# Kernel tuning notes

Hardware: AMD Instinct MI355X
Metric: run time of the kernel (lower is better)

Reference implementation:

```python
import jax, jax.numpy as jnp
import numpy as np

N_HEADS = 16
N_KV = 8
HEAD_DIM = 128
HID = 2048
GROUPS = N_HEADS // N_KV
THETA = 10000.0


def _rope_cos_sin(position_ids, dtype):
    # position_ids: [1, S] int
    inv_freq = 1.0 / (THETA ** (jnp.arange(0, HEAD_DIM, 2, dtype=jnp.float32) / HEAD_DIM))
    freqs = position_ids.astype(jnp.float32)[:, :, None] * inv_freq[None, None, :]  # [1,S,hd/2]
    emb = jnp.concatenate([freqs, freqs], axis=-1)  # [1,S,hd]
    return jnp.cos(emb).astype(dtype)[:, None, :, :], jnp.sin(emb).astype(dtype)[:, None, :, :]


def _rotate_half(x):
    x1, x2 = x[..., : HEAD_DIM // 2], x[..., HEAD_DIM // 2 :]
    return jnp.concatenate([-x2, x1], axis=-1)


def setup_inputs() -> dict:
    key = jax.random.key(0)
    ks = jax.random.split(key, 8)
    B, S = 2, 2048
    hidden_states = jax.random.normal(ks[0], (B, S, HID), jnp.float32)
    Wq = jax.random.normal(ks[1], (HID, N_HEADS * HEAD_DIM), jnp.float32) * 0.02
    Wk = jax.random.normal(ks[2], (HID, N_KV * HEAD_DIM), jnp.float32) * 0.02
    Wv = jax.random.normal(ks[3], (HID, N_KV * HEAD_DIM), jnp.float32) * 0.02
    Wo = jax.random.normal(ks[4], (HID, HID), jnp.float32) * 0.02
    gate = jnp.zeros((1, N_HEADS, 1, 1), jnp.float32)
    memory_in = jax.random.normal(ks[5], (B, N_KV, HEAD_DIM, HEAD_DIM), jnp.float32)
    norm_in = jax.random.uniform(ks[6], (B, N_KV, 1, HEAD_DIM), jnp.float32)
    position_ids = jnp.arange(S, dtype=jnp.int32)[None, :]
    return {"hidden_states": hidden_states, "Wq": Wq, "Wk": Wk, "Wv": Wv, "Wo": Wo,
            "gate": gate, "memory_in": memory_in, "norm_in": norm_in,
            "position_ids": position_ids}


def reference(hidden_states, Wq, Wk, Wv, Wo, gate, memory_in, norm_in, position_ids):
    B, S, _ = hidden_states.shape
    # projections -> [B, H, S, hd]
    q = jnp.einsum('bsh,ho->bso', hidden_states, Wq).reshape(B, S, N_HEADS, HEAD_DIM).transpose(0, 2, 1, 3)
    k = jnp.einsum('bsh,ho->bso', hidden_states, Wk).reshape(B, S, N_KV, HEAD_DIM).transpose(0, 2, 1, 3)
    v = jnp.einsum('bsh,ho->bso', hidden_states, Wv).reshape(B, S, N_KV, HEAD_DIM).transpose(0, 2, 1, 3)

    # ---- compressive memory retrieval (pre-RoPE q, as in original) ----
    sigma_q = jax.nn.elu(q) + 1.0  # [B, nH, S, hd]
    mem_tiled = jnp.tile(memory_in, (1, GROUPS, 1, 1))          # torch .repeat tiles
    norm_tiled = jnp.tile(norm_in, (1, GROUPS, 1, 1))            # [B, nH, 1, hd]
    memory_output = jnp.einsum('bhsd,bhde->bhse', sigma_q, mem_tiled)
    norm_bcast = jnp.einsum('bhsd,bhd->bhs', sigma_q, norm_tiled[:, :, 0, :])[..., None]
    memory_output = memory_output / norm_bcast

    # ---- memory update (pre-RoPE k, v) ----
    sigma_k = jax.nn.elu(k) + 1.0  # [B, nKV, S, hd]
    updated_memory = memory_in + jnp.einsum('bhsd,bhse->bhde', sigma_k, v)
    updated_norm = norm_in + jnp.sum(sigma_k, axis=2, keepdims=True)

    # ---- RoPE ----
    cos, sin = _rope_cos_sin(position_ids, q.dtype)
    q = q * cos + _rotate_half(q) * sin
    k = k * cos + _rotate_half(k) * sin

    # ---- repeat_kv (interleave, groups) ----
    k = jnp.repeat(k, GROUPS, axis=1)
    v = jnp.repeat(v, GROUPS, axis=1)

    # ---- causal SDPA ----
    scale = 1.0 / np.sqrt(HEAD_DIM)
    scores = jnp.einsum('bhqd,bhkd->bhqk', q, k) * scale
    causal = jnp.tril(jnp.ones((S, S), dtype=bool))
    scores = jnp.where(causal[None, None], scores, jnp.finfo(scores.dtype).min)
    probs = jax.nn.softmax(scores, axis=-1)
    attn = jnp.einsum('bhqk,bhkd->bhqd', probs, v)

    # ---- gated combination + output projection ----
    g = jax.nn.sigmoid(gate)
    combined = g * memory_output + (1.0 - g) * attn  # [B, nH, S, hd]
    combined = combined.transpose(0, 2, 1, 3).reshape(B, S, HID)
    final_output = jnp.einsum('bsh,ho->bso', combined, Wo)
    return final_output, updated_memory, updated_norm
```

## Files before the change

### kernel.cpp

```cpp
#include <hip/hip_runtime.h>

#define BATCH 2
#define SEQ   2048
#define HID   2048
#define NH    16
#define NKV   8
#define HD    128
#define M_ROWS (BATCH * SEQ)
#define QKV_N  4096

typedef __attribute__((ext_vector_type(8))) __bf16 bf16x8;
typedef __attribute__((ext_vector_type(4))) float  f32x4;

static __device__ __forceinline__ f32x4 mfma16(bf16x8 a, bf16x8 b, f32x4 c) {
    return __builtin_amdgcn_mfma_f32_16x16x32_bf16(a, b, c, 0, 0, 0);
}
static __device__ __forceinline__ float sigma_f(float x) {
    return x > 0.f ? x + 1.f : __expf(x);
}
static __device__ __forceinline__ void gload16(const __bf16* g, __bf16* l) {
    __builtin_amdgcn_global_load_lds(
        (const __attribute__((address_space(1))) void*)g,
        (__attribute__((address_space(3))) void*)l, 16, 0, 0);
}

#define OFF_QKV  0ull
#define OFF_SQ   67108864ull
#define OFF_QR   83886080ull
#define OFF_KR   100663296ull
#define OFF_VT   109051904ull
#define OFF_ND   117440512ull
#define OFF_CB   117702656ull
#define OFF_PART 134479872ull
#define OFF_BND  142868480ull
#define OFF_MAXP 143130624ull
#define OFF_NPART 143134720ull
#define NSPLIT 8

__global__ void f2b_k(const float* __restrict__ src, __bf16* __restrict__ dst)
{
    const size_t i = ((size_t)blockIdx.x * 256 + threadIdx.x) * 8;
    const float4 v0 = *reinterpret_cast<const float4*>(src + i);
    const float4 v1 = *reinterpret_cast<const float4*>(src + i + 4);
    bf16x8 t;
    t[0]=(__bf16)v0.x; t[1]=(__bf16)v0.y; t[2]=(__bf16)v0.z; t[3]=(__bf16)v0.w;
    t[4]=(__bf16)v1.x; t[5]=(__bf16)v1.y; t[6]=(__bf16)v1.z; t[7]=(__bf16)v1.w;
    *reinterpret_cast<bf16x8*>(dst + i) = t;
}

__global__ __launch_bounds__(256) void tr_k(const float* __restrict__ W,
                                            __bf16* __restrict__ Bt, int K, int N)
{
    __shared__ __bf16 T[64][72];
    const int k0 = blockIdx.x * 64, n0 = blockIdx.y * 64;
    const int t = threadIdx.x;
    #pragma unroll
    for (int i = 0; i < 4; ++i) {
        const int idx = t + i * 256;
        const int r = idx >> 4, c4 = (idx & 15) * 4;
        const float4 v = *reinterpret_cast<const float4*>(&W[(size_t)(k0 + r) * N + n0 + c4]);
        T[c4 + 0][r] = (__bf16)v.x; T[c4 + 1][r] = (__bf16)v.y;
        T[c4 + 2][r] = (__bf16)v.z; T[c4 + 3][r] = (__bf16)v.w;
    }
    __syncthreads();
    #pragma unroll
    for (int i = 0; i < 2; ++i) {
        const int idx = t + i * 256;
        const int rr = idx >> 3, cc = (idx & 7) * 8;
        *reinterpret_cast<bf16x8*>(&Bt[(size_t)(n0 + rr) * K + k0 + cc]) =
            *reinterpret_cast<bf16x8*>(&T[rr][cc]);
    }
}

__global__ __launch_bounds__(512, 2) void gemm8_k(const __bf16* __restrict__ A,
                                                  const __bf16* __restrict__ Bt,
                                                  float* __restrict__ C,
                                                  int N, int K)
{
    __shared__ __align__(16) __bf16 smem[65536];
    const int tid = threadIdx.x, wave = tid >> 6, lane = tid & 63;
    const int l15 = lane & 15, l4 = lane >> 4;
    const int wr = wave >> 2, wc = wave & 3;

    const int nwg = gridDim.x;
    const int swz = (blockIdx.x & 7) * (nwg >> 3) + (blockIdx.x >> 3);
    const int NBN = N >> 8;
    const int bm = swz / NBN, bn = swz - bm * NBN;
    const int m0 = bm << 8, n0 = bn << 8;

    const int NKT = K >> 6;

    const int srow   = tid >> 2;
    const int schunk = (tid & 3) ^ ((tid >> 3) & 3);
    const int sdst   = wave * 512;

    const int achunk = l4 ^ ((l15 >> 1) & 3);
    const int aoff = (wr * 128 + l15) * 32 + achunk * 8;
    const int boff = (wc * 64  + l15) * 32 + achunk * 8;

    f32x4 acc[2][4][4] = {};
    bf16x8 af[4], bfr[4];

#define STAGE_SLAB(gb, r0, koff, slabptr) do {                                   \
        const __bf16* _g = (gb) + (size_t)((r0) + srow) * K + (koff) + schunk * 8; \
        gload16(_g,                    (slabptr) + sdst);                        \
        gload16(_g + (size_t)128 * K,  (slabptr) + sdst + 4096);                 \
    } while (0)

    STAGE_SLAB(A,  m0, 0,  smem);
    STAGE_SLAB(Bt, n0, 0,  smem + 16384);
    STAGE_SLAB(A,  m0, 32, smem + 8192);
    STAGE_SLAB(Bt, n0, 32, smem + 24576);
    STAGE_SLAB(A,  m0, 64, smem + 32768);
    STAGE_SLAB(Bt, n0, 64, smem + 32768 + 16384);
    asm volatile("s_waitcnt vmcnt(4)" ::: "memory");
    __builtin_amdgcn_s_barrier();

    #pragma unroll 1
    for (int T = 0; T < NKT; ++T) {
        __bf16* bufc = smem + (T & 1) * 32768;
        __bf16* bufn = smem + ((T & 1) ^ 1) * 32768;
        const int kt1 = (T + 1) * 64, kt2 = (T + 2) * 64;

        {
            const __bf16* As = bufc;
            const __bf16* Bs = bufc + 16384;
            #pragma unroll
            for (int f = 0; f < 4; ++f)  af[f]  = *reinterpret_cast<const bf16x8*>(As + aoff + f * 512);
            #pragma unroll
            for (int nf = 0; nf < 4; ++nf) bfr[nf] = *reinterpret_cast<const bf16x8*>(Bs + boff + nf * 512);
            if (T + 1 < NKT) STAGE_SLAB(A, m0, kt1 + 32, bufn + 8192);
            __builtin_amdgcn_s_barrier();
            __builtin_amdgcn_s_setprio(1);
            #pragma unroll
            for (int f = 0; f < 4; ++f)
                #pragma unroll
                for (int nf = 0; nf < 4; ++nf)
                    acc[0][f][nf] = mfma16(af[f], bfr[nf], acc[0][f][nf]);
            __builtin_amdgcn_s_setprio(0);
            __builtin_amdgcn_s_barrier();
        }
        {
            const __bf16* As = bufc;
            #pragma unroll
            for (int f = 0; f < 4; ++f)  af[f] = *reinterpret_cast<const bf16x8*>(As + aoff + 2048 + f * 512);
            if (T + 1 < NKT) STAGE_SLAB(Bt, n0, kt1 + 32, bufn + 24576);
            __builtin_amdgcn_s_barrier();
            __builtin_amdgcn_s_setprio(1);
            #pragma unroll
            for (int f = 0; f < 4; ++f)
                #pragma unroll
                for (int nf = 0; nf < 4; ++nf)
                    acc[1][f][nf] = mfma16(af[f], bfr[nf], acc[1][f][nf]);
            __builtin_amdgcn_s_setprio(0);
            __builtin_amdgcn_s_barrier();
        }
        {
            const __bf16* As = bufc + 8192;
            const __bf16* Bs = bufc + 24576;
            #pragma unroll
            for (int f = 0; f < 4; ++f)  af[f]  = *reinterpret_cast<const bf16x8*>(As + aoff + f * 512);
            #pragma unroll
            for (int nf = 0; nf < 4; ++nf) bfr[nf] = *reinterpret_cast<const bf16x8*>(Bs + boff + nf * 512);
            if (T + 2 < NKT) STAGE_SLAB(A, m0, kt2, bufc);
            __builtin_amdgcn_s_barrier();
            __builtin_amdgcn_s_setprio(1);
            #pragma unroll
            for (int f = 0; f < 4; ++f)
                #pragma unroll
                for (int nf = 0; nf < 4; ++nf)
                    acc[0][f][nf] = mfma16(af[f], bfr[nf], acc[0][f][nf]);
            __builtin_amdgcn_s_setprio(0);
            __builtin_amdgcn_s_barrier();
        }
        {
            const __bf16* As = bufc + 8192;
            #pragma unroll
            for (int f = 0; f < 4; ++f)  af[f] = *reinterpret_cast<const bf16x8*>(As + aoff + 2048 + f * 512);
            if (T + 2 < NKT) STAGE_SLAB(Bt, n0, kt2, bufc + 16384);
            __builtin_amdgcn_s_barrier();
            __builtin_amdgcn_s_setprio(1);
            #pragma unroll
            for (int f = 0; f < 4; ++f)
                #pragma unroll
                for (int nf = 0; nf < 4; ++nf)
                    acc[1][f][nf] = mfma16(af[f], bfr[nf], acc[1][f][nf]);
            __builtin_amdgcn_s_setprio(0);
            if (T < NKT - 2) asm volatile("s_waitcnt vmcnt(4)" ::: "memory");
            else             asm volatile("s_waitcnt vmcnt(0)" ::: "memory");
            __builtin_amdgcn_s_barrier();
        }
    }
#undef STAGE_SLAB

    #pragma unroll
    for (int mh = 0; mh < 2; ++mh)
        #pragma unroll
        for (int f = 0; f < 4; ++f)
            #pragma unroll
            for (int nf = 0; nf < 4; ++nf)
                #pragma unroll
                for (int r = 0; r < 4; ++r) {
                    const int row = m0 + wr * 128 + mh * 64 + f * 16 + l4 * 4 + r;
                    const int col = n0 + wc * 64 + nf * 16 + l15;
                    C[(size_t)row * N + col] = acc[mh][f][nf][r];
                }
}

__global__ __launch_bounds__(256) void prep_k(const float* __restrict__ qkv,
                                              const float* __restrict__ norm_in,
                                              const int* __restrict__ pos_ids,
                                              __bf16* __restrict__ sq, __bf16* __restrict__ qr,
                                              __bf16* __restrict__ kr, __bf16* __restrict__ vt,
                                              float* __restrict__ nd, float* __restrict__ bnd,
                                              float* __restrict__ maxp)
{
    const int sc = blockIdx.x, kvh = blockIdx.y, b = blockIdx.z;
    const int s0 = sc * 32, t = threadIdx.x;
    const float scale = 0.08838834764831845f;
    const float s2 = scale * scale;
    const float NEG_LN_TH = -0.14391156831212787f;
    __shared__ float krn[32];

    {
        const int row = t >> 2;
        const int head = row >> 5, sl = row & 31;
        const int hq = kvh * 2 + head, nh = hq & 7;
        const int dq = (t & 3) * 16;
        const int pos = pos_ids[s0 + sl];
        const float* qp = qkv + (size_t)(b * SEQ + s0 + sl) * QKV_N + hq * 128;
        const float* np = norm_in + (b * NKV + nh) * 128;

        float x0[16], x1[16];
        #pragma unroll
        for (int i = 0; i < 16; i += 4) {
            *reinterpret_cast<float4*>(&x0[i]) = *reinterpret_cast<const float4*>(qp + dq + i);
            *reinterpret_cast<float4*>(&x1[i]) = *reinterpret_cast<const float4*>(qp + dq + 64 + i);
        }
        float nds = 0.f, qns = 0.f;
        bf16x8 sqv0[2], sqv1[2], qrv0[2], qrv1[2];
        #pragma unroll
        for (int i = 0; i < 16; ++i) {
            const int j = dq + i;
            float c, sn;
            __sincosf((float)pos * __expf((float)j * NEG_LN_TH), &sn, &c);
            qrv0[i >> 3][i & 7] = (__bf16)((x0[i] * c - x1[i] * sn) * scale);
            qrv1[i >> 3][i & 7] = (__bf16)((x1[i] * c + x0[i] * sn) * scale);
            const float sg0 = sigma_f(x0[i]), sg1 = sigma_f(x1[i]);
            sqv0[i >> 3][i & 7] = (__bf16)sg0;
            sqv1[i >> 3][i & 7] = (__bf16)sg1;
            nds += sg0 * np[j] + sg1 * np[j + 64];
            qns += (x0[i] * x0[i] + x1[i] * x1[i]) * s2;
        }
        __bf16* sqp = sq + ((size_t)(b * NH + hq) * SEQ + s0 + sl) * 128;
        __bf16* qrp = qr + ((size_t)(b * NH + hq) * SEQ + s0 + sl) * 128;
        *reinterpret_cast<bf16x8*>(sqp + dq)      = sqv0[0];
        *reinterpret_cast<bf16x8*>(sqp + dq + 8)  = sqv0[1];
        *reinterpret_cast<bf16x8*>(sqp + dq + 64) = sqv1[0];
        *reinterpret_cast<bf16x8*>(sqp + dq + 72) = sqv1[1];
        *reinterpret_cast<bf16x8*>(qrp + dq)      = qrv0[0];
        *reinterpret_cast<bf16x8*>(qrp + dq + 8)  = qrv0[1];
        *reinterpret_cast<bf16x8*>(qrp + dq + 64) = qrv1[0];
        *reinterpret_cast<bf16x8*>(qrp + dq + 72) = qrv1[1];

        nds += __shfl_xor(nds, 1); nds += __shfl_xor(nds, 2);
        qns += __shfl_xor(qns, 1); qns += __shfl_xor(qns, 2);
        if ((t & 3) == 0) {
            nd [(size_t)(b * NH + hq) * SEQ + s0 + sl] = nds;
            bnd[(size_t)(b * NH + hq) * SEQ + s0 + sl] = qns;
        }
    }

    if (t < 128) {
        const int sl = t >> 2;
        const int dq = (t & 3) * 16;
        const int pos = pos_ids[s0 + sl];
        const float* kp = qkv + (size_t)(b * SEQ + s0 + sl) * QKV_N + 2048 + kvh * 128;
        float x0[16], x1[16];
        #pragma unroll
        for (int i = 0; i < 16; i += 4) {
            *reinterpret_cast<float4*>(&x0[i]) = *reinterpret_cast<const float4*>(kp + dq + i);
            *reinterpret_cast<float4*>(&x1[i]) = *reinterpret_cast<const float4*>(kp + dq + 64 + i);
        }
        bf16x8 kv0[2], kv1[2];
        float kns = 0.f;
        #pragma unroll
        for (int i = 0; i < 16; ++i) {
            const int j = dq + i;
            float c, sn;
            __sincosf((float)pos * __expf((float)j * NEG_LN_TH), &sn, &c);
            kv0[i >> 3][i & 7] = (__bf16)(x0[i] * c - x1[i] * sn);
            kv1[i >> 3][i & 7] = (__bf16)(x1[i] * c + x0[i] * sn);
            kns += x0[i] * x0[i] + x1[i] * x1[i];
        }
        __bf16* krp = kr + ((size_t)(b * NKV + kvh) * SEQ + s0 + sl) * 128;
        *reinterpret_cast<bf16x8*>(krp + dq)      = kv0[0];
        *reinterpret_cast<bf16x8*>(krp + dq + 8)  = kv0[1];
        *reinterpret_cast<bf16x8*>(krp + dq + 64) = kv1[0];
        *reinterpret_cast<bf16x8*>(krp + dq + 72) = kv1[1];
        kns += __shfl_xor(kns, 1); kns += __shfl_xor(kns, 2);
        if ((t & 3) == 0) krn[sl] = kns;
    }

    __shared__ float vl[128][33];
    {
        const int sl = t >> 3, dch = (t & 7) * 16;
        const float* vp = qkv + (size_t)(b * SEQ + s0 + sl) * QKV_N + 3072 + kvh * 128 + dch;
        float xv[16];
        #pragma unroll
        for (int i = 0; i < 16; i += 4)
            *reinterpret_cast<float4*>(&xv[i]) = *reinterpret_cast<const float4*>(vp + i);
        #pragma unroll
        for (int i = 0; i < 16; ++i) vl[dch + i][sl] = xv[i];
    }
    __syncthreads();
    if (t == 0) {
        float mx = 0.f;
        #pragma unroll
        for (int i = 0; i < 32; ++i) mx = fmaxf(mx, krn[i]);
        maxp[((b * NKV + kvh) << 6) + sc] = mx;
    }
    {
        const int d = t >> 1, sh = (t & 1) * 16;
        bf16x8 o0, o1;
        #pragma unroll
        for (int j = 0; j < 8; ++j) o0[j] = (__bf16)vl[d][sh + j];
        #pragma unroll
        for (int j = 0; j < 8; ++j) o1[j] = (__bf16)vl[d][sh + 8 + j];
        __bf16* vp = vt + ((size_t)((b * NKV + kvh) * 128 + d)) * SEQ + s0 + sh;
        *reinterpret_cast<bf16x8*>(vp)     = o0;
        *reinterpret_cast<bf16x8*>(vp + 8) = o1;
    }
}

__global__ __launch_bounds__(256) void memout_k(const __bf16* __restrict__ sq,
                                                const float* __restrict__ mem_in,
                                                const float* __restrict__ nd,
                                                const float* __restrict__ gate,
                                                __bf16* __restrict__ cb)
{
    __shared__ __align__(16) __bf16 mt[128][136];
    const int tid = threadIdx.x;
    const int h = blockIdx.y, b = blockIdx.z;
    const int s0 = blockIdx.x * 64;

    const float* mem = mem_in + (size_t)(b * NKV + (h & 7)) * 16384;
    for (int i = tid; i < 16384; i += 256) {
        int dd = i >> 7, e = i & 127;
        mt[e][dd] = (__bf16)mem[i];
    }
    __syncthreads();

    const int wave = tid >> 6, lane = tid & 63, l15 = lane & 15, l4 = lane >> 4;
    f32x4 acc[8] = {};
    const __bf16* sqb = sq + ((size_t)(b * NH + h) * SEQ + s0 + wave * 16 + l15) * 128;
    #pragma unroll
    for (int kb = 0; kb < 4; ++kb) {
        bf16x8 a = *reinterpret_cast<const bf16x8*>(sqb + kb * 32 + l4 * 8);
        #pragma unroll
        for (int nc = 0; nc < 8; ++nc) {
            bf16x8 bb = *reinterpret_cast<bf16x8*>(&mt[nc * 16 + l15][kb * 32 + l4 * 8]);
            acc[nc] = mfma16(a, bb, acc[nc]);
        }
    }
    float g = 1.f / (1.f + __expf(-gate[h]));
    #pragma unroll
    for (int r = 0; r < 4; ++r) {
        int srow = s0 + wave * 16 + l4 * 4 + r;
        float scl = g / nd[(size_t)(b * NH + h) * SEQ + srow];
        __bf16* cbp = cb + (size_t)(b * SEQ + srow) * HID + h * 128;
        #pragma unroll
        for (int nc = 0; nc < 8; ++nc)
            cbp[nc * 16 + l15] = (__bf16)(acc[nc][r] * scl);
    }
}

__global__ __launch_bounds__(256) void memupd_k(const float* __restrict__ qkv,
                                                float* __restrict__ part,
                                                float* __restrict__ npart)
{
    const int sp = blockIdx.x, h = blockIdx.y, b = blockIdx.z;
    const int tid = threadIdx.x;
    const int tx = tid & 15, ty = tid >> 4;
    __shared__ __align__(16) float sk[8][128];
    __shared__ __align__(16) float sv[8][128];
    float acc[8][8] = {};
    float nacc = 0.f;

    const int s0 = sp * (SEQ / NSPLIT);
    for (int so = 0; so < SEQ / NSPLIT; so += 8) {
        for (int i = tid; i < 8 * 128; i += 256) {
            int rr = i >> 7, dd = i & 127;
            const float* rowp = qkv + (size_t)(b * SEQ + s0 + so + rr) * QKV_N;
            sk[rr][dd] = sigma_f(rowp[2048 + h * 128 + dd]);
            sv[rr][dd] = rowp[3072 + h * 128 + dd];
        }
        __syncthreads();
        if (tid < 128) {
            #pragma unroll
            for (int rr = 0; rr < 8; ++rr) nacc += sk[rr][tid];
        }
        #pragma unroll
        for (int rr = 0; rr < 8; ++rr) {
            float4 k0 = *reinterpret_cast<float4*>(&sk[rr][tx * 8]);
            float4 k1 = *reinterpret_cast<float4*>(&sk[rr][tx * 8 + 4]);
            float4 v0 = *reinterpret_cast<float4*>(&sv[rr][ty * 8]);
            float4 v1 = *reinterpret_cast<float4*>(&sv[rr][ty * 8 + 4]);
            float kreg[8] = {k0.x,k0.y,k0.z,k0.w,k1.x,k1.y,k1.z,k1.w};
            float vreg[8] = {v0.x,v0.y,v0.z,v0.w,v1.x,v1.y,v1.z,v1.w};
            #pragma unroll
            for (int i = 0; i < 8; ++i)
                #pragma unroll
                for (int j2 = 0; j2 < 8; ++j2)
                    acc[i][j2] += kreg[i] * vreg[j2];
        }
        __syncthreads();
    }
    float* pb = part + ((size_t)sp * (BATCH * NKV) + b * NKV + h) * 16384;
    #pragma unroll
    for (int i = 0; i < 8; ++i)
        #pragma unroll
        for (int j2 = 0; j2 < 8; ++j2)
            pb[(tx * 8 + i) * 128 + ty * 8 + j2] = acc[i][j2];
    if (tid < 128)
        npart[((size_t)sp * (BATCH * NKV) + b * NKV + h) * 128 + tid] = nacc;
}

__global__ void memred_k(const float* __restrict__ part, const float* __restrict__ mem_in,
                         float* __restrict__ out_mem)
{
    const size_t i = (size_t)blockIdx.x * 256 + threadIdx.x;
    float a = mem_in[i];
    #pragma unroll
    for (int sp = 0; sp < NSPLIT; ++sp) a += part[(size_t)sp * 262144 + i];
    out_mem[i] = a;
}

__global__ void normred_k(const float* __restrict__ npart, const float* __restrict__ norm_in,
                          float* __restrict__ out_norm)
{
    const int bh = blockIdx.x, d = threadIdx.x;
    float a = norm_in[bh * 128 + d];
    #pragma unroll
    for (int sp = 0; sp < NSPLIT; ++sp)
        a += npart[((size_t)sp * (BATCH * NKV) + bh) * 128 + d];
    out_norm[bh * 128 + d] = a;
}

__global__ __launch_bounds__(256, 2) void attn_k(const __bf16* __restrict__ qr,
                                                 const __bf16* __restrict__ kr,
                                                 const __bf16* __restrict__ vt,
                                                 const float* __restrict__ gate,
                                                 const float* __restrict__ bnd,
                                                 const float* __restrict__ maxp,
                                                 __bf16* __restrict__ cb)
{
    __shared__ __align__(16) char smem[81920];
    __bf16* Ks   = (__bf16*)smem;
    __bf16* Vs   = (__bf16*)(smem + 32768);
    __bf16* plds = (__bf16*)(smem + 65536);
    float*  red  = (float*)smem;
    float*  lred = (float*)(smem + 65536);

    const int tid = threadIdx.x, wave = tid >> 6, lane = tid & 63;
    const int l15 = lane & 15, l4 = lane >> 4;

    const int n   = blockIdx.x + 16 * (blockIdx.y + 16 * blockIdx.z);
    const int xcd = n & 7, i64 = n >> 3;
    const int grp = xcd * 2 + (i64 >> 5);
    const int within = i64 & 31;
    const int b   = grp >> 3;
    const int kvh = grp & 7;
    const int h   = kvh * 2 + (within >> 4);
    const int x   = within & 15;

    const __bf16* kbase = kr + (size_t)(b * NKV + kvh) * SEQ * 128;
    const __bf16* vbase = vt + (size_t)(b * NKV + kvh) * 128 * SEQ;
    const float* bbase  = bnd + (size_t)(b * NH + h) * SEQ;

    const float g  = 1.f / (1.f + __expf(-gate[h]));
    const float gi = 1.f - g;
    float kn2 = 0.f;
    const float* mp = maxp + (b * NKV + kvh) * 64;
    #pragma unroll
    for (int i = 0; i < 64; i += 4) {
        const float4 v = *reinterpret_cast<const float4*>(mp + i);
        kn2 = fmaxf(kn2, fmaxf(fmaxf(v.x, v.y), fmaxf(v.z, v.w)));
    }
    const float knmax = sqrtf(kn2);

    bf16x8 ones;
    #pragma unroll
    for (int j = 0; j < 8; ++j) ones[j] = (__bf16)1.0f;

    const int srow = wave * 32 + (lane >> 4);
    __bf16* ksd = Ks + wave * 4096;
    __bf16* vsd = Vs + wave * 4096;

    __bf16* pw = plds + wave * 2048;
    const int ksub = wave >> 1;
    const int wq   = wave & 1;

    #pragma unroll 1
    for (int tile = 0; tile < 2; ++tile) {
        const int q0 = (tile == 0 ? x : 31 - x) * 64;
        const int qw = q0 + wq * 32;
        const int NT = (q0 >> 6) + 1;
        const int NI = (NT + 1) >> 1;

        bf16x8 af[2][4];
        float m_r[2][4];
        #pragma unroll
        for (int m = 0; m < 2; ++m) {
            const __bf16* qb = qr + ((size_t)(b * NH + h) * SEQ + qw + m * 16 + l15) * 128;
            #pragma unroll
            for (int kb = 0; kb < 4; ++kb)
                af[m][kb] = *reinterpret_cast<const bf16x8*>(qb + kb * 32 + l4 * 8);
            #pragma unroll
            for (int r = 0; r < 4; ++r)
                m_r[m][r] = sqrtf(bbase[qw + m * 16 + l4 * 4 + r]) * knmax + 1.0f;
        }

        f32x4 o0[8] = {}, o1[8] = {};
        f32x4 lc0 = {}, lc1 = {};

        #pragma unroll 1
        for (int it = 0; it < NI; ++it) {
            const int kt0 = it * 128;
            #pragma unroll
            for (int j = 0; j < 8; ++j) {
                const int row = srow + j * 4;
                const int ch  = (lane & 15) ^ (row & 7);
                gload16(kbase + (size_t)(kt0 + row) * 128 + ch * 8, ksd + j * 512);
                gload16(vbase + (size_t)row * SEQ + kt0 + ch * 8,   vsd + j * 512);
            }
            __syncthreads();

            const int s = 2 * it + ksub;
            if (s < NT) {
                const int krow0 = ksub * 64;
                f32x4 s0[4] = {}, s1[4] = {};
                #pragma unroll
                for (int kb = 0; kb < 4; ++kb) {
                    #pragma unroll
                    for (int sub = 0; sub < 4; ++sub) {
                        const int krow = krow0 + sub * 16 + l15;
                        bf16x8 bb = *reinterpret_cast<const bf16x8*>(
                            Ks + krow * 128 + (((kb * 4 + l4) ^ (krow & 7)) * 8));
                        s0[sub] = mfma16(af[0][kb], bb, s0[sub]);
                        s1[sub] = mfma16(af[1][kb], bb, s1[sub]);
                    }
                }
                #pragma unroll
                for (int r = 0; r < 4; ++r) {
                    const int q0r = qw + l4 * 4 + r;
                    const int q1r = q0r + 16;
                    const int p0r = l4 * 4 + r, p1r = p0r + 16;
                    #pragma unroll
                    for (int sub = 0; sub < 4; ++sub) {
                        const int key = s * 64 + sub * 16 + l15;
                        float p0 = __expf(s0[sub][r] - m_r[0][r]);
                        float p1 = __expf(s1[sub][r] - m_r[1][r]);
                        p0 = (key <= q0r) ? p0 : 0.f;
                        p1 = (key <= q1r) ? p1 : 0.f;
                        const int cc = (sub * 16 + l15) >> 3, cl = l15 & 7;
                        pw[p0r * 64 + ((cc ^ (p0r & 7)) * 8) + cl] = (__bf16)p0;
                        pw[p1r * 64 + ((cc ^ (p1r & 7)) * 8) + cl] = (__bf16)p1;
                    }
                }
                const int pr1 = 16 + l15;
                bf16x8 a00 = *reinterpret_cast<bf16x8*>(pw + l15 * 64 + ((l4 ^ (l15 & 7)) * 8));
                bf16x8 a01 = *reinterpret_cast<bf16x8*>(pw + l15 * 64 + (((4 + l4) ^ (l15 & 7)) * 8));
                bf16x8 a10 = *reinterpret_cast<bf16x8*>(pw + pr1 * 64 + ((l4 ^ (pr1 & 7)) * 8));
                bf16x8 a11 = *reinterpret_cast<bf16x8*>(pw + pr1 * 64 + (((4 + l4) ^ (pr1 & 7)) * 8));
                lc0 = mfma16(a00, ones, lc0); lc0 = mfma16(a01, ones, lc0);
                lc1 = mfma16(a10, ones, lc1); lc1 = mfma16(a11, ones, lc1);
                #pragma unroll
                for (int nc = 0; nc < 8; ++nc) {
                    const int vrow = nc * 16 + l15;
                    bf16x8 b0 = *reinterpret_cast<bf16x8*>(
                        Vs + vrow * 128 + (((ksub * 8 + l4) ^ (vrow & 7)) * 8));
                    bf16x8 b1 = *reinterpret_cast<bf16x8*>(
                        Vs + vrow * 128 + (((ksub * 8 + 4 + l4) ^ (vrow & 7)) * 8));
                    o0[nc] = mfma16(a00, b0, o0[nc]); o0[nc] = mfma16(a01, b1, o0[nc]);
                    o1[nc] = mfma16(a10, b0, o1[nc]); o1[nc] = mfma16(a11, b1, o1[nc]);
                }
            }
            __syncthreads();
        }

        if (wave >= 2) {
            float* rb = red + (wave - 2) * 4224;
            #pragma unroll
            for (int nc = 0; nc < 8; ++nc)
                #pragma unroll
                for (int r = 0; r < 4; ++r) {
                    rb[(l4 * 4 + r) * 132 + nc * 16 + l15]        = o0[nc][r];
                    rb[(16 + l4 * 4 + r) * 132 + nc * 16 + l15]   = o1[nc][r];
                }
            if (l15 == 0) {
                float* lb = lred + (wave - 2) * 32;
                #pragma unroll
                for (int r = 0; r < 4; ++r) {
                    lb[l4 * 4 + r]      = lc0[r];
                    lb[16 + l4 * 4 + r] = lc1[r];
                }
            }
        }
        __syncthreads();
        if (wave < 2) {
            float* rb = red + wave * 4224;
            const float* lb = lred + wave * 32;
            #pragma unroll
            for (int r = 0; r < 4; ++r) {
                const int qrow = qw + l4 * 4 + r;
                const float i0 = gi / (lc0[r] + lb[l4 * 4 + r]);
                const float i1 = gi / (lc1[r] + lb[16 + l4 * 4 + r]);
                __bf16* c0 = cb + (size_t)(b * SEQ + qrow) * HID + h * 128;
                __bf16* c1 = cb + (size_t)(b * SEQ + qrow + 16) * HID + h * 128;
                #pragma unroll
                for (int nc = 0; nc < 8; ++nc) {
                    const int dd = nc * 16 + l15;
                    const float v0 = o0[nc][r] + rb[(l4 * 4 + r) * 132 + dd];
                    const float v1 = o1[nc][r] + rb[(16 + l4 * 4 + r) * 132 + dd];
                    c0[dd] = (__bf16)((float)c0[dd] + v0 * i0);
                    c1[dd] = (__bf16)((float)c1[dd] + v1 * i1);
                }
            }
        }
        __syncthreads();
    }
}

extern "C" void kernel_launch(void* const* d_in, const int* in_sizes, int n_in,
                              void* d_out, int out_size, void* d_ws, size_t ws_size,
                              hipStream_t stream)
{
    const float* hidden  = (const float*)d_in[0];
    const float* Wq      = (const float*)d_in[1];
    const float* Wk      = (const float*)d_in[2];
    const float* Wv      = (const float*)d_in[3];
    const float* Wo      = (const float*)d_in[4];
    const float* gate    = (const float*)d_in[5];
    const float* mem_in  = (const float*)d_in[6];
    const float* norm_in = (const float*)d_in[7];
    const int*   pos     = (const int*)d_in[8];

    float* out_final = (float*)d_out;
    float* out_mem   = out_final + (size_t)BATCH * SEQ * HID;
    float* out_norm  = out_mem + (size_t)BATCH * NKV * 128 * 128;

    char* ws = (char*)d_ws;
    float*  qkv  = (float*)(ws + OFF_QKV);
    __bf16* sq   = (__bf16*)(ws + OFF_SQ);
    __bf16* qrb  = (__bf16*)(ws + OFF_QR);
    __bf16* krb  = (__bf16*)(ws + OFF_KR);
    __bf16* vtb  = (__bf16*)(ws + OFF_VT);
    float*  nd   = (float*)(ws + OFF_ND);
    __bf16* cb   = (__bf16*)(ws + OFF_CB);
    float*  part = (float*)(ws + OFF_PART);
    float*  bnd  = (float*)(ws + OFF_BND);
    float*  maxp = (float*)(ws + OFF_MAXP);
    float*  npart = (float*)(ws + OFF_NPART);
    __bf16* hb   = (__bf16*)(ws + OFF_SQ);
    __bf16* qkvT = (__bf16*)(ws + OFF_QR);
    __bf16* woT  = (__bf16*)(ws + OFF_PART);

    f2b_k<<<(M_ROWS * HID) / (256 * 8), 256, 0, stream>>>(hidden, hb);
    tr_k<<<dim3(HID / 64, 2048 / 64), 256, 0, stream>>>(Wq, qkvT, HID, 2048);
    tr_k<<<dim3(HID / 64, 1024 / 64), 256, 0, stream>>>(Wk, qkvT + (size_t)2048 * HID, HID, 1024);
    tr_k<<<dim3(HID / 64, 1024 / 64), 256, 0, stream>>>(Wv, qkvT + (size_t)3072 * HID, HID, 1024);

    gemm8_k<<<(M_ROWS / 256) * (QKV_N / 256), 512, 0, stream>>>(hb, qkvT, qkv, QKV_N, HID);

    prep_k<<<dim3(SEQ / 32, NKV, BATCH), 256, 0, stream>>>(qkv, norm_in, pos, sq, qrb, krb, vtb,
                                                           nd, bnd, maxp);

    memout_k<<<dim3(SEQ / 64, NH, BATCH), 256, 0, stream>>>(sq, mem_in, nd, gate, cb);

    memupd_k<<<dim3(NSPLIT, NKV, BATCH), 256, 0, stream>>>(qkv, part, npart);
    memred_k<<<(BATCH * NKV * 128 * 128) / 256, 256, 0, stream>>>(part, mem_in, out_mem);
    normred_k<<<BATCH * NKV, 128, 0, stream>>>(npart, norm_in, out_norm);

    tr_k<<<dim3(HID / 64, HID / 64), 256, 0, stream>>>(Wo, woT, HID, HID);

    attn_k<<<dim3(16, NH, BATCH), 256, 0, stream>>>(qrb, krb, vtb, gate, bnd, maxp, cb);

    gemm8_k<<<(M_ROWS / 256) * (HID / 256), 512, 0, stream>>>(cb, woT, out_final, HID, HID);
}
```

Before: 462.7 us.

## Software-pipeline K/V tile loads in attention kernel with split waitcnts and swizzle

Restructures the attention inner loop so the next K tile is issued right after the QK^T MFMAs and the next V tile after the PV MFMAs. Explicit vmcnt waits and raw s_barriers replace the single load-then-syncthreads pattern, so global-to-LDS traffic overlaps with compute. It also precomputes swizzled byte offsets for K, V and P accesses, adds setprio around MFMA blocks, and changes the P scratch layout. This adds more barriers per iteration and relies on hand-counted vmcnt values, which could be fragile.

```diff
diff --git a/kernel.cpp b/kernel.cpp
--- a/kernel.cpp
+++ b/kernel.cpp
@@ -456,14 +456,17 @@
                                                  __bf16* __restrict__ cb)
 {
     __shared__ __align__(16) char smem[81920];
-    __bf16* Ks   = (__bf16*)smem;
-    __bf16* Vs   = (__bf16*)(smem + 32768);
-    __bf16* plds = (__bf16*)(smem + 65536);
+    char* ksB = smem;
+    char* vsB = smem + 32768;
+    char* pB  = smem + 65536;
     float*  red  = (float*)smem;
     float*  lred = (float*)(smem + 65536);
 
     const int tid = threadIdx.x, wave = tid >> 6, lane = tid & 63;
     const int l15 = lane & 15, l4 = lane >> 4;
+    const int e3 = l15 & 7, e2 = e3 >> 2;
+    const int ksub = wave >> 1;
+    const int wq   = wave & 1;
 
     const int n   = blockIdx.x + 16 * (blockIdx.y + 16 * blockIdx.z);
     const int xcd = n & 7, i64 = n >> 3;
@@ -493,13 +496,37 @@
     #pragma unroll
     for (int j = 0; j < 8; ++j) ones[j] = (__bf16)1.0f;
 
-    const int srow = wave * 32 + (lane >> 4);
-    __bf16* ksd = Ks + wave * 4096;
-    __bf16* vsd = Vs + wave * 4096;
-
-    __bf16* pw = plds + wave * 2048;
-    const int ksub = wave >> 1;
-    const int wq   = wave & 1;
+    const int srow = wave * 32 + l4;
+    const int chA  = (lane & 15) ^ l4;
+    const char* KG0 = (const char*)kbase + srow * 256 + chA * 16;
+    const char* KG1 = (const char*)kbase + srow * 256 + ((chA ^ 4) * 16);
+    const char* VG0 = (const char*)vbase + srow * 4096 + chA * 16;
+    const char* VG1 = (const char*)vbase + srow * 4096 + ((chA ^ 4) * 16);
+    __bf16* kdst = (__bf16*)(ksB + wave * 8192);
+    __bf16* vdst = (__bf16*)(vsB + wave * 8192);
+
+    const int t16 = (l4 ^ (e3 & 3)) * 16;
+    const int KBe = l15 * 256 + ksub * 16384 + t16 + e2 * 64;
+    const int KBo = l15 * 256 + ksub * 16384 + t16 + (1 ^ e2) * 64;
+    const int VB0 = l15 * 256 + t16 + e2 * 64 + ksub * 128;
+    const int VB1 = l15 * 256 + t16 + (1 ^ e2) * 64 + ksub * 128;
+    const int PWw = wave * 4096 + l4 * 512 + l15 * 2;
+    const int PWr = wave * 4096 + l15 * 128 + l4 * 16;
+
+#define ISSUE_K(ktrow) do {                                                      \
+        const int _ko = (ktrow) * 256;                                           \
+        _Pragma("unroll")                                                        \
+        for (int _j = 0; _j < 8; ++_j)                                           \
+            gload16((const __bf16*)(((_j & 1) ? KG1 : KG0) + _ko + _j * 1024),   \
+                    kdst + _j * 512);                                            \
+    } while (0)
+#define ISSUE_V(ktrow) do {                                                      \
+        const int _vo = (ktrow) * 2;                                             \
+        _Pragma("unroll")                                                        \
+        for (int _j = 0; _j < 8; ++_j)                                           \
+            gload16((const __bf16*)(((_j & 1) ? VG1 : VG0) + _vo + _j * 16384),  \
+                    vdst + _j * 512);                                            \
+    } while (0)
 
     #pragma unroll 1
     for (int tile = 0; tile < 2; ++tile) {
@@ -524,38 +551,43 @@
         f32x4 o0[8] = {}, o1[8] = {};
         f32x4 lc0 = {}, lc1 = {};
 
+        ISSUE_K(0);
+        ISSUE_V(0);
+        asm volatile("s_waitcnt vmcnt(8)" ::: "memory");
+        __builtin_amdgcn_sched_barrier(0);
+        __builtin_amdgcn_s_barrier();
+
         #pragma unroll 1
         for (int it = 0; it < NI; ++it) {
-            const int kt0 = it * 128;
-            #pragma unroll
-            for (int j = 0; j < 8; ++j) {
-                const int row = srow + j * 4;
-                const int ch  = (lane & 15) ^ (row & 7);
-                gload16(kbase + (size_t)(kt0 + row) * 128 + ch * 8, ksd + j * 512);
-                gload16(vbase + (size_t)row * SEQ + kt0 + ch * 8,   vsd + j * 512);
-            }
-            __syncthreads();
-
             const int s = 2 * it + ksub;
-            if (s < NT) {
-                const int krow0 = ksub * 64;
-                f32x4 s0[4] = {}, s1[4] = {};
+            const bool act  = (s < NT);
+            const bool more = (it + 1 < NI);
+
+            f32x4 s0[4] = {}, s1[4] = {};
+            if (act) {
+                __builtin_amdgcn_s_setprio(1);
                 #pragma unroll
                 for (int kb = 0; kb < 4; ++kb) {
+                    const int kbb = ((kb & 1) ? KBo : KBe) + (kb >> 1) * 128;
                     #pragma unroll
                     for (int sub = 0; sub < 4; ++sub) {
-                        const int krow = krow0 + sub * 16 + l15;
-                        bf16x8 bb = *reinterpret_cast<const bf16x8*>(
-                            Ks + krow * 128 + (((kb * 4 + l4) ^ (krow & 7)) * 8));
+                        bf16x8 bb = *reinterpret_cast<const bf16x8*>(ksB + kbb + sub * 4096);
                         s0[sub] = mfma16(af[0][kb], bb, s0[sub]);
                         s1[sub] = mfma16(af[1][kb], bb, s1[sub]);
                     }
                 }
+                __builtin_amdgcn_s_setprio(0);
+            }
+            __builtin_amdgcn_sched_barrier(0);
+            __builtin_amdgcn_s_barrier();
+
+            if (more) ISSUE_K((it + 1) * 128);
+
+            if (act) {
                 #pragma unroll
                 for (int r = 0; r < 4; ++r) {
                     const int q0r = qw + l4 * 4 + r;
                     const int q1r = q0r + 16;
-                    const int p0r = l4 * 4 + r, p1r = p0r + 16;
                     #pragma unroll
                     for (int sub = 0; sub < 4; ++sub) {
                         const int key = s * 64 + sub * 16 + l15;
@@ -563,30 +595,44 @@
                         float p1 = __expf(s1[sub][r] - m_r[1][r]);
                         p0 = (key <= q0r) ? p0 : 0.f;
                         p1 = (key <= q1r) ? p1 : 0.f;
-                        const int cc = (sub * 16 + l15) >> 3, cl = l15 & 7;
-                        pw[p0r * 64 + ((cc ^ (p0r & 7)) * 8) + cl] = (__bf16)p0;
-                        pw[p1r * 64 + ((cc ^ (p1r & 7)) * 8) + cl] = (__bf16)p1;
+                        *(__bf16*)(pB + PWw + r * 128 + sub * 32)        = (__bf16)p0;
+                        *(__bf16*)(pB + PWw + 2048 + r * 128 + sub * 32) = (__bf16)p1;
                     }
                 }
-                const int pr1 = 16 + l15;
-                bf16x8 a00 = *reinterpret_cast<bf16x8*>(pw + l15 * 64 + ((l4 ^ (l15 & 7)) * 8));
-                bf16x8 a01 = *reinterpret_cast<bf16x8*>(pw + l15 * 64 + (((4 + l4) ^ (l15 & 7)) * 8));
-                bf16x8 a10 = *reinterpret_cast<bf16x8*>(pw + pr1 * 64 + ((l4 ^ (pr1 & 7)) * 8));
-                bf16x8 a11 = *reinterpret_cast<bf16x8*>(pw + pr1 * 64 + (((4 + l4) ^ (pr1 & 7)) * 8));
+            }
+            if (more) asm volatile("s_waitcnt vmcnt(8)" ::: "memory");
+            else      asm volatile("s_waitcnt vmcnt(0)" ::: "memory");
+            __builtin_amdgcn_sched_barrier(0);
+            __builtin_amdgcn_s_barrier();
+
+            if (act) {
+                bf16x8 a00 = *reinterpret_cast<const bf16x8*>(pB + PWr);
+                bf16x8 a01 = *reinterpret_cast<const bf16x8*>(pB + PWr + 64);
+                bf16x8 a10 = *reinterpret_cast<const bf16x8*>(pB + PWr + 2048);
+                bf16x8 a11 = *reinterpret_cast<const bf16x8*>(pB + PWr + 2048 + 64);
+                __builtin_amdgcn_s_setprio(1);
                 lc0 = mfma16(a00, ones, lc0); lc0 = mfma16(a01, ones, lc0);
                 lc1 = mfma16(a10, ones, lc1); lc1 = mfma16(a11, ones, lc1);
                 #pragma unroll
                 for (int nc = 0; nc < 8; ++nc) {
-                    const int vrow = nc * 16 + l15;
-                    bf16x8 b0 = *reinterpret_cast<bf16x8*>(
-                        Vs + vrow * 128 + (((ksub * 8 + l4) ^ (vrow & 7)) * 8));
-                    bf16x8 b1 = *reinterpret_cast<bf16x8*>(
-                        Vs + vrow * 128 + (((ksub * 8 + 4 + l4) ^ (vrow & 7)) * 8));
+                    bf16x8 b0 = *reinterpret_cast<const bf16x8*>(vsB + VB0 + nc * 4096);
+                    bf16x8 b1 = *reinterpret_cast<const bf16x8*>(vsB + VB1 + nc * 4096);
                     o0[nc] = mfma16(a00, b0, o0[nc]); o0[nc] = mfma16(a01, b1, o0[nc]);
                     o1[nc] = mfma16(a10, b0, o1[nc]); o1[nc] = mfma16(a11, b1, o1[nc]);
                 }
+                __builtin_amdgcn_s_setprio(0);
             }
-            __syncthreads();
+            __builtin_amdgcn_sched_barrier(0);
+            __builtin_amdgcn_s_barrier();
+
+            if (more) {
+                ISSUE_V((it + 1) * 128);
+                asm volatile("s_waitcnt vmcnt(8)" ::: "memory");
+            } else {
+                asm volatile("s_waitcnt vmcnt(0)" ::: "memory");
+            }
+            __builtin_amdgcn_sched_barrier(0);
+            __builtin_amdgcn_s_barrier();
         }
 
         if (wave >= 2) {
@@ -630,6 +676,8 @@
         }
         __syncthreads();
     }
+#undef ISSUE_K
+#undef ISSUE_V
 }
 
 extern "C" void kernel_launch(void* const* d_in, const int* in_sizes, int n_in,
```

After: 470.3 us. No clear change (+1.6%).
